# Kernel optimization log

Measured on AMD Instinct MI355X. Metric: run time of the kernel, lower is better.

## Reference

```python
import jax, jax.numpy as jnp
import numpy as np
from jax import lax

BITWIDTH = 7
EPS = 1e-5


def ti_quant(x):
    """TiFloatToInt8: per-tensor int8 quantization with power-of-2 scale."""
    rng = jnp.max(jnp.abs(x))
    bw = jnp.ceil(jnp.log2(rng))
    exp = bw - BITWIDTH
    q = jnp.clip(jnp.round(x * 2.0 ** (BITWIDTH - bw)), -128.0, 127.0)
    return q, exp


def ti_conv(xv, xe, wv, we, pad):
    """TiConv2d: integer conv (simulated in f32, all values int-valued),
    int32 accumulate, then shift back to 8 bits; exponents add."""
    acc = lax.conv_general_dilated(
        xv, wv, window_strides=(1, 1), padding=[(pad, pad), (pad, pad)],
        dimension_numbers=("NCHW", "OIHW", "NCHW"))
    rng = jnp.max(jnp.abs(acc))
    bw = jnp.ceil(jnp.log2(rng))
    shift = jnp.maximum(bw - BITWIDTH, 0.0)
    q = jnp.clip(jnp.round(acc * 2.0 ** (-shift)), -128.0, 127.0)
    return q, xe + we + shift


def batchnorm(x, gamma, beta):
    # training-mode BN: batch statistics over (N, H, W)
    mean = jnp.mean(x, axis=(0, 2, 3), keepdims=True)
    var = jnp.var(x, axis=(0, 2, 3), keepdims=True)
    g = gamma[None, :, None, None]
    b = beta[None, :, None, None]
    return g * (x - mean) * lax.rsqrt(var + EPS) + b


def setup_inputs() -> dict:
    key = jax.random.key(0)
    k0, k1, k2, k3, k4 = jax.random.split(key, 5)
    B, Cin, Cout, H, W = 32, 128, 256, 56, 56
    x_val = jax.random.randint(k0, (B, Cin, H, W), -128, 128, dtype=jnp.int32)
    x_exp = jnp.zeros((), jnp.float32) - 7.0
    wDW = jnp.round(jnp.clip(jax.random.normal(k1, (Cin, Cin, 3, 3), jnp.float32) * 32.0, -128.0, 127.0))
    wDW_exp = jnp.zeros((), jnp.float32) - 9.0
    wPW = jnp.round(jnp.clip(jax.random.normal(k2, (Cout, Cin, 1, 1), jnp.float32) * 32.0, -128.0, 127.0))
    wPW_exp = jnp.zeros((), jnp.float32) - 9.0
    gamma1 = jnp.ones((Cin,), jnp.float32) + 0.1 * jax.random.normal(k3, (Cin,), jnp.float32)
    beta1 = jnp.zeros((Cin,), jnp.float32)
    gamma2 = jnp.ones((Cout,), jnp.float32) + 0.1 * jax.random.normal(k4, (Cout,), jnp.float32)
    beta2 = jnp.zeros((Cout,), jnp.float32)
    return {"x_val": x_val, "x_exp": x_exp, "wDW": wDW, "wDW_exp": wDW_exp,
            "wPW": wPW, "wPW_exp": wPW_exp, "gamma1": gamma1, "beta1": beta1,
            "gamma2": gamma2, "beta2": beta2}


def reference(x_val, x_exp, wDW, wDW_exp, wPW, wPW_exp, gamma1, beta1, gamma2, beta2):
    xv = x_val.astype(jnp.float32)
    # convDW (3x3, in->in, pad=1)
    q, e = ti_conv(xv, x_exp, wDW, wDW_exp, 1)
    # dequant -> bn1 -> quant
    f = batchnorm(q * 2.0 ** e, gamma1, beta1)
    q, e = ti_quant(f)
    # TiReLU on int values
    q = jnp.maximum(q, 0.0)
    # convPW (1x1, in->out)
    q, e = ti_conv(q, e, wPW, wPW_exp, 0)
    # dequant -> bn2 -> quant -> relu
    f = batchnorm(q * 2.0 ** e, gamma2, beta2)
    q, e = ti_quant(f)
    q = jnp.maximum(q, 0.0)
    return q.astype(jnp.int8), e
```

## Files before the change

kernel.cpp:

```cpp
#include <hip/hip_runtime.h>
#include <cstdint>
#include <cstddef>

#define C1 128
#define C2 256
#define Hh 56
#define Wd 56
#define HW 3136
#define NHW 100352
#define N1 ((size_t)12845056)
#define N2 ((size_t)25690112)
#define XPSZ ((size_t)13778944)
#define NREP 8

typedef int v4i __attribute__((ext_vector_type(4)));
typedef int v16i __attribute__((ext_vector_type(16)));

static constexpr size_t OFF_XP = 0;
static constexpr size_t OFF_ACC1 = XPSZ;
static constexpr size_t OFF_Q1 = OFF_ACC1 + 4 * N1;
static constexpr size_t OFF_Q3 = OFF_Q1 + N1;
static constexpr size_t OFF_WQ1 = OFF_Q3 + N2;
static constexpr size_t OFF_WQ2 = OFF_WQ1 + 147456;
static constexpr size_t OFF_STATS = OFF_WQ2 + 32768;

struct Stats {
  int absmax1, absmax2, tick1, tick2;
  float scale1, e1, s2, e2;
  float scaleq2, e3, sf, ef;
  int sum1[NREP][C1]; unsigned sumsq1[NREP][C1];
  int min1[NREP][C1], max1[NREP][C1];
  float A1[C1], B1c[C1];
  int sum2[NREP][C2]; unsigned sumsq2[NREP][C2];
  int min2[NREP][C2], max2[NREP][C2];
  float A2[C2], B2c[C2];
};

__global__ __launch_bounds__(256) void k_pre(
    const int* __restrict__ x, signed char* __restrict__ xp,
    const float* __restrict__ wDW, signed char* __restrict__ wq1t,
    const float* __restrict__ wPW, signed char* __restrict__ wq2t,
    Stats* st) {
  __shared__ signed char lds[56 * 132];
  int t = threadIdx.x, bid = blockIdx.x;
  if (bid < 1856) {
    int hh = bid % 58, n = bid / 58;
    int* xpw = (int*)(xp + ((size_t)n * 58 + hh) * 7424);
    if (hh == 0 || hh == 57) {
      for (int o = t; o < 1856; o += 256) xpw[o] = 0;
      return;
    }
    int h = hh - 1;
    const int* xb = x + (size_t)n * C1 * HW + h * 56;
    for (int idx = t; idx < 7168; idx += 256) {
      int c = idx / 56, w = idx - c * 56;
      lds[w * 132 + c] = (signed char)xb[(size_t)c * HW + w];
    }
    __syncthreads();
    for (int o = t; o < 1856; o += 256) {
      int kb = o / 232, r = o - kb * 232, ww = r >> 2, cw = r & 3;
      int val = (ww == 0 || ww == 57) ? 0
                : *(const int*)&lds[(ww - 1) * 132 + kb * 16 + cw * 4];
      xpw[o] = val;
    }
    return;
  }
  if (bid < 2432) {
    int idx = (bid - 1856) * 256 + t;
    int co = idx / 1152, r = idx - co * 1152;
    int ci = r / 9, pos = r - ci * 9;
    int k = pos * 128 + ci;
    wq1t[(size_t)(k >> 4) * 2048 + co * 16 + (k & 15)] = (signed char)(int)wDW[idx];
    return;
  }
  if (bid < 2560) {
    int i = (bid - 2432) * 256 + t;
    int co = i >> 7, ci = i & 127;
    wq2t[(size_t)(ci >> 4) * 4096 + co * 16 + (ci & 15)] = (signed char)(int)wPW[i];
    return;
  }
  if (t == 0) { st->absmax1 = 0; st->absmax2 = 0; st->tick1 = 0; st->tick2 = 0; }
  for (int c = t; c < NREP * C1; c += 256) {
    ((int*)st->sum1)[c] = 0; ((unsigned*)st->sumsq1)[c] = 0u;
    ((int*)st->min1)[c] = 127; ((int*)st->max1)[c] = -128;
  }
  for (int c = t; c < NREP * C2; c += 256) {
    ((int*)st->sum2)[c] = 0; ((unsigned*)st->sumsq2)[c] = 0u;
    ((int*)st->min2)[c] = 127; ((int*)st->max2)[c] = -128;
  }
}

__device__ inline v4i ld16_lds(const signed char* p) {
  const int2* q = (const int2*)p;
  int2 lo = q[0], hi = q[1];
  v4i r; r[0] = lo.x; r[1] = lo.y; r[2] = hi.x; r[3] = hi.y;
  return r;
}

__device__ inline float bn_affine_v(int sum, unsigned sumsq, int mn, int mx,
                                    float g, float b, float e_in,
                                    float* Aout, float* Bout) {
  double meanq = (double)sum / (double)NHW;
  double varq = (double)sumsq / (double)NHW - meanq * meanq;
  float se = exp2f(e_in);
  float mean = (float)meanq * se;
  float var = (float)varq * se * se;
  float rsq = 1.0f / sqrtf(var + 1e-5f);
  float Avv = g * se * rsq;
  float Bvv = b - g * mean * rsq;
  *Aout = Avv; *Bout = Bvv;
  return fmaxf(fabsf(Avv * (float)mn + Bvv), fabsf(Avv * (float)mx + Bvv));
}

__global__ __launch_bounds__(256, 2) void k_conv1s(
    const signed char* __restrict__ xp, const signed char* __restrict__ wq1t,
    int* __restrict__ acc1, Stats* st) {
  __shared__ int reda[4];
  int t = threadIdx.x, lane = t & 63, wave = t >> 6;
  int half = lane >> 5, l31 = lane & 31;
  size_t g0 = (size_t)blockIdx.x * 256;

  const signed char* ab[2];
#pragma unroll
  for (int i = 0; i < 2; ++i) {
    size_t gm = g0 + wave * 64 + i * 32 + l31;
    int n = (int)(gm / HW);
    int p = (int)(gm - (size_t)n * HW);
    int h = p / 56, w = p - h * 56;
    ab[i] = xp + ((size_t)n * 58 + h) * 7424 + w * 16 + half * 928;
  }
  const signed char* bb[4];
#pragma unroll
  for (int j = 0; j < 4; ++j)
    bb[j] = wq1t + (size_t)(j * 32 + l31) * 16 + half * 2048;

  v16i a1[2][4];
#pragma unroll
  for (int i = 0; i < 2; ++i)
#pragma unroll
    for (int j = 0; j < 4; ++j)
#pragma unroll
      for (int r = 0; r < 16; ++r) a1[i][j][r] = 0;

#pragma unroll
  for (int pos = 0; pos < 9; ++pos) {
    int kh = pos / 3, kw = pos - kh * 3;
    const signed char* a0p = ab[0] + kh * 7424 + kw * 16;
    const signed char* a1p = ab[1] + kh * 7424 + kw * 16;
#pragma unroll
    for (int kb = 0; kb < 8; kb += 2) {
      v4i af0 = *(const v4i*)(a0p + kb * 928);
      v4i af1 = *(const v4i*)(a1p + kb * 928);
      v4i bf[4];
#pragma unroll
      for (int j = 0; j < 4; ++j)
        bf[j] = *(const v4i*)(bb[j] + pos * 16384 + kb * 2048);
#pragma unroll
      for (int j = 0; j < 4; ++j) {
        a1[0][j] = __builtin_amdgcn_mfma_i32_32x32x32_i8(af0, bf[j], a1[0][j], 0, 0, 0);
        a1[1][j] = __builtin_amdgcn_mfma_i32_32x32x32_i8(af1, bf[j], a1[1][j], 0, 0, 0);
      }
    }
  }

  int am = 0;
#pragma unroll
  for (int i = 0; i < 2; ++i)
#pragma unroll
    for (int j = 0; j < 4; ++j)
#pragma unroll
      for (int r = 0; r < 16; ++r) am = max(am, abs(a1[i][j][r]));
  for (int off = 32; off; off >>= 1) am = max(am, __shfl_down(am, off, 64));
  if (lane == 0) reda[wave] = am;
  __syncthreads();
  if (t == 0)
    atomicMax(&st->absmax1, max(max(reda[0], reda[1]), max(reda[2], reda[3])));

  int* ob = acc1 + (size_t)blockIdx.x * 32768;
#pragma unroll
  for (int i = 0; i < 2; ++i)
#pragma unroll
    for (int j = 0; j < 4; ++j)
#pragma unroll
      for (int reg = 0; reg < 16; ++reg)
        ob[(((wave * 2 + i) * 4 + j) * 16 + reg) * 64 + lane] = a1[i][j][reg];
}

__global__ __launch_bounds__(256, 2) void k_qstats1(
    const int* __restrict__ acc1, signed char* __restrict__ q1, Stats* st,
    const float* __restrict__ x_exp, const float* __restrict__ wDW_exp,
    const float* __restrict__ gamma1, const float* __restrict__ beta1) {
  __shared__ int qti[256 * 34];
  __shared__ int psum[C1], psq[C1], pmn[C1], pmx[C1];
  __shared__ float redc[2];
  __shared__ int lastf;
  signed char* qt = (signed char*)qti;
  int t = threadIdx.x, lane = t & 63, wave = t >> 6;
  int half = lane >> 5, l31 = lane & 31;
  int rep = blockIdx.x & (NREP - 1);

  if (t < C1) { psum[t] = 0; psq[t] = 0; pmn[t] = 127; pmx[t] = -128; }
  __syncthreads();

  int v1 = st->absmax1;
  int pw = 31 - __clz(v1 | 1);
  int bw = ((v1 & (v1 - 1)) == 0) ? pw : pw + 1;
  int sh = max(bw - 7, 0);
  float scale1 = exp2f((float)(-sh));
  float e1 = x_exp[0] + wDW_exp[0] + (float)sh;
  if (blockIdx.x == 0 && t == 0) st->e1 = e1;

  const int* ib = acc1 + (size_t)blockIdx.x * 32768;
#pragma unroll
  for (int j = 0; j < 4; ++j) {
    int sj = 0, sqj = 0, mnj = 127, mxj = -128;
    int c = j * 32 + l31;
#pragma unroll
    for (int i = 0; i < 2; ++i)
#pragma unroll
      for (int reg = 0; reg < 16; ++reg) {
        int av = ib[(((wave * 2 + i) * 4 + j) * 16 + reg) * 64 + lane];
        int row = (reg & 3) + 8 * (reg >> 2) + 4 * half;
        int pix = wave * 64 + i * 32 + row;
        float r = rintf((float)av * scale1);
        r = fminf(fmaxf(r, -128.f), 127.f);
        int qi = (int)r;
        qt[pix * 136 + c] = (signed char)qi;
        sj += qi; sqj += qi * qi; mnj = min(mnj, qi); mxj = max(mxj, qi);
      }
    sj += __shfl_down(sj, 32, 64);
    sqj += __shfl_down(sqj, 32, 64);
    mnj = min(mnj, __shfl_down(mnj, 32, 64));
    mxj = max(mxj, __shfl_down(mxj, 32, 64));
    if (half == 0) {
      atomicAdd(&psum[c], sj); atomicAdd(&psq[c], sqj);
      atomicMin(&pmn[c], mnj); atomicMax(&pmx[c], mxj);
    }
  }
  __syncthreads();
  if (t < C1) {
    atomicAdd(&st->sum1[rep][t], psum[t]);
    atomicAdd(&st->sumsq1[rep][t], (unsigned)psq[t]);
    atomicMin(&st->min1[rep][t], pmn[t]);
    atomicMax(&st->max1[rep][t], pmx[t]);
  }
  int* q1w = (int*)(q1 + (size_t)blockIdx.x * 256 * 128);
  for (int idx = t; idx < 8192; idx += 256)
    q1w[idx] = qti[(idx >> 5) * 34 + (idx & 31)];

  __syncthreads();
  if (t == 0) lastf = (atomicAdd(&st->tick1, 1) == 391);
  __syncthreads();
  if (lastf) {
    if (t < C1) {
      int sm = 0; unsigned sq = 0; int mn = 127, mx = -128;
#pragma unroll
      for (int r2 = 0; r2 < NREP; ++r2) {
        sm += atomicAdd(&st->sum1[r2][t], 0);
        sq += atomicAdd(&st->sumsq1[r2][t], 0u);
        mn = min(mn, atomicMin(&st->min1[r2][t], 127));
        mx = max(mx, atomicMax(&st->max1[r2][t], -128));
      }
      float cand = bn_affine_v(sm, sq, mn, mx, gamma1[t], beta1[t], e1,
                               &st->A1[t], &st->B1c[t]);
      for (int off = 32; off; off >>= 1) cand = fmaxf(cand, __shfl_down(cand, off, 64));
      if ((t & 63) == 0) redc[t >> 6] = cand;
    }
    __syncthreads();
    if (t == 0) {
      float rng = fmaxf(redc[0], redc[1]);
      float bwv = ceilf(log2f(rng));
      st->s2 = exp2f(7.0f - bwv);
      st->e2 = bwv - 7.0f;
    }
  }
}

template <int STORE>
__global__ __launch_bounds__(256, 2) void k_conv2t(
    const signed char* __restrict__ q1, const signed char* __restrict__ wq2t,
    signed char* __restrict__ q3, Stats* st, const float* __restrict__ wPW_exp,
    const float* __restrict__ gamma2, const float* __restrict__ beta2,
    float* __restrict__ out) {
  __shared__ __align__(16) signed char wq2s[32768];
  __shared__ int qti[128 * 34];
  __shared__ int psum[C2], psq[C2], pmn[C2], pmx[C2];
  __shared__ int reda[4];
  __shared__ float red2[4];
  __shared__ int lastf;
  signed char* qt = (signed char*)qti;

  int t = threadIdx.x, lane = t & 63, wave = t >> 6;
  int half = lane >> 5, l31 = lane & 31;
  size_t g0 = (size_t)blockIdx.x * 128;
  int rep = blockIdx.x & (NREP - 1);

  v4i wtmp[8];
#pragma unroll
  for (int i = 0; i < 8; ++i)
    wtmp[i] = *(const v4i*)(wq2t + i * 4096 + t * 16);
  const int* q1w = (const int*)(q1 + g0 * 128);
  int qv[16];
#pragma unroll
  for (int k = 0; k < 16; ++k) qv[k] = q1w[k * 256 + t];

  if (STORE) { psum[t] = 0; psq[t] = 0; pmn[t] = 127; pmx[t] = -128; }

  int c4 = t & 31;
  float Av[4], Bv[4];
#pragma unroll
  for (int jj = 0; jj < 4; ++jj) {
    Av[jj] = st->A1[c4 * 4 + jj];
    Bv[jj] = st->B1c[c4 * 4 + jj];
  }
  float s2 = st->s2;

#pragma unroll
  for (int i = 0; i < 8; ++i)
    *(v4i*)(wq2s + i * 4096 + t * 16) = wtmp[i];

#pragma unroll
  for (int k = 0; k < 16; ++k) {
    int v = qv[k];
    int pix = (k * 256 + t) >> 5;
    int outv = 0;
#pragma unroll
    for (int jj = 0; jj < 4; ++jj) {
      int b = (signed char)(v >> (8 * jj));
      float y = Av[jj] * (float)b + Bv[jj];
      float r = rintf(y * s2);
      r = fminf(fmaxf(r, -128.f), 127.f);
      r = fmaxf(r, 0.f);
      outv |= ((int)r & 0xff) << (8 * jj);
    }
    qti[pix * 34 + c4] = outv;
  }
  __syncthreads();

  v16i acc[8];
#pragma unroll
  for (int j = 0; j < 8; ++j)
#pragma unroll
    for (int r = 0; r < 16; ++r) acc[j][r] = 0;

#pragma unroll
  for (int ks = 0; ks < 4; ++ks) {
    v4i af = ld16_lds(&qt[(wave * 32 + l31) * 136 + half * 16 + ks * 32]);
#pragma unroll
    for (int j = 0; j < 8; ++j) {
      v4i bf = *(const v4i*)(wq2s + (size_t)(ks * 2 + half) * 4096 + (j * 32 + l31) * 16);
      acc[j] = __builtin_amdgcn_mfma_i32_32x32x32_i8(af, bf, acc[j], 0, 0, 0);
    }
  }

  if (STORE == 0) {
    int am2 = 0;
#pragma unroll
    for (int j = 0; j < 8; ++j)
#pragma unroll
      for (int r = 0; r < 16; ++r) am2 = max(am2, abs(acc[j][r]));
    for (int off = 32; off; off >>= 1) am2 = max(am2, __shfl_down(am2, off, 64));
    if (lane == 0) reda[wave] = am2;
    __syncthreads();
    if (t == 0)
      atomicMax(&st->absmax2, max(max(reda[0], reda[1]), max(reda[2], reda[3])));
  } else {
    int v2 = st->absmax2;
    int pw = 31 - __clz(v2 | 1);
    int bw = ((v2 & (v2 - 1)) == 0) ? pw : pw + 1;
    int sh2 = max(bw - 7, 0);
    float scale2 = exp2f((float)(-sh2));
    float e3 = st->e2 + wPW_exp[0] + (float)sh2;
    if (blockIdx.x == 0 && t == 0) st->e3 = e3;
    int* q3w = (int*)(q3 + (size_t)blockIdx.x * 32768);
#pragma unroll
    for (int j = 0; j < 8; ++j) {
      int c = j * 32 + l31;
      int sj = 0, sqj = 0, mnj = 127, mxj = -128;
#pragma unroll
      for (int rg = 0; rg < 4; ++rg) {
        int pk = 0;
#pragma unroll
        for (int b = 0; b < 4; ++b) {
          float r = rintf((float)acc[j][4 * rg + b] * scale2);
          r = fminf(fmaxf(r, -128.f), 127.f);
          int qi = (int)r;
          pk |= (qi & 0xff) << (8 * b);
          sj += qi; sqj += qi * qi; mnj = min(mnj, qi); mxj = max(mxj, qi);
        }
        q3w[((wave * 8 + j) * 4 + rg) * 64 + lane] = pk;
      }
      sj += __shfl_down(sj, 32, 64);
      sqj += __shfl_down(sqj, 32, 64);
      mnj = min(mnj, __shfl_down(mnj, 32, 64));
      mxj = max(mxj, __shfl_down(mxj, 32, 64));
      if (half == 0) {
        atomicAdd(&psum[c], sj); atomicAdd(&psq[c], sqj);
        atomicMin(&pmn[c], mnj); atomicMax(&pmx[c], mxj);
      }
    }
    __syncthreads();
    atomicAdd(&st->sum2[rep][t], psum[t]);
    atomicAdd(&st->sumsq2[rep][t], (unsigned)psq[t]);
    atomicMin(&st->min2[rep][t], pmn[t]);
    atomicMax(&st->max2[rep][t], pmx[t]);

    __syncthreads();
    if (t == 0) lastf = (atomicAdd(&st->tick2, 1) == 783);
    __syncthreads();
    if (lastf) {
      int sm = 0; unsigned sq = 0; int mn = 127, mx = -128;
#pragma unroll
      for (int r2 = 0; r2 < NREP; ++r2) {
        sm += atomicAdd(&st->sum2[r2][t], 0);
        sq += atomicAdd(&st->sumsq2[r2][t], 0u);
        mn = min(mn, atomicMin(&st->min2[r2][t], 127));
        mx = max(mx, atomicMax(&st->max2[r2][t], -128));
      }
      float cand = bn_affine_v(sm, sq, mn, mx, gamma2[t], beta2[t], e3,
                               &st->A2[t], &st->B2c[t]);
      for (int off = 32; off; off >>= 1) cand = fmaxf(cand, __shfl_down(cand, off, 64));
      if (lane == 0) red2[wave] = cand;
      __syncthreads();
      if (t == 0) {
        float rng = fmaxf(fmaxf(red2[0], red2[1]), fmaxf(red2[2], red2[3]));
        float bwv = ceilf(log2f(rng));
        st->sf = exp2f(7.0f - bwv);
        st->ef = bwv - 7.0f;
        out[N2] = bwv - 7.0f;
      }
    }
  }
}

__global__ __launch_bounds__(256) void k_out(
    const signed char* __restrict__ q3, const Stats* __restrict__ st,
    float* __restrict__ out) {
  __shared__ int ldsc[256 * 17];
  int t = threadIdx.x, lane = t & 63, wave = t >> 6;
  int bid = blockIdx.x;
  size_t g0 = (size_t)bid * 64;
  int n = (int)(g0 / HW), p0 = (int)(g0 - (size_t)n * HW);
  const int* q3r = (const int*)(q3 + (size_t)(bid >> 1) * 32768) + (bid & 1) * 4096;
#pragma unroll
  for (int k = 0; k < 16; ++k) {
    int i = k * 256 + t;
    int ln = i & 63, rg = (i >> 6) & 3, j = (i >> 8) & 7, wv = (i >> 11) & 1;
    int v = q3r[i];
    int c = j * 32 + (ln & 31);
    int psub = wv * 8 + 2 * rg + (ln >> 5);
    ldsc[c * 17 + psub] = v;
  }
  __syncthreads();
  float sf = st->sf;
  float* ob = out + (size_t)n * C2 * HW + p0 + lane;
#pragma unroll
  for (int cg = 0; cg < 64; ++cg) {
    int c = wave * 64 + ((cg + wave * 16) & 63);
    int vv = ldsc[c * 17 + (lane >> 2)];
    float y = st->A2[c] * (float)((signed char)(vv >> (8 * (lane & 3)))) + st->B2c[c];
    float r = rintf(y * sf);
    r = fminf(fmaxf(r, -128.f), 127.f);
    ob[(size_t)c * HW] = fmaxf(r, 0.f);
  }
}

extern "C" void kernel_launch(void* const* d_in, const int* in_sizes, int n_in,
                              void* d_out, int out_size, void* d_ws, size_t ws_size,
                              hipStream_t stream) {
  const int* x = (const int*)d_in[0];
  const float* x_exp = (const float*)d_in[1];
  const float* wDW = (const float*)d_in[2];
  const float* wDW_exp = (const float*)d_in[3];
  const float* wPW = (const float*)d_in[4];
  const float* wPW_exp = (const float*)d_in[5];
  const float* gamma1 = (const float*)d_in[6];
  const float* beta1 = (const float*)d_in[7];
  const float* gamma2 = (const float*)d_in[8];
  const float* beta2 = (const float*)d_in[9];
  float* out = (float*)d_out;

  char* ws = (char*)d_ws;
  signed char* xp2 = (signed char*)(ws + OFF_XP);
  int* acc1 = (int*)(ws + OFF_ACC1);
  signed char* q1 = (signed char*)(ws + OFF_Q1);
  signed char* q3 = (signed char*)(ws + OFF_Q3);
  signed char* wq1t = (signed char*)(ws + OFF_WQ1);
  signed char* wq2t = (signed char*)(ws + OFF_WQ2);
  Stats* st = (Stats*)(ws + OFF_STATS);

  hipLaunchKernelGGL(k_pre, dim3(2561), dim3(256), 0, stream,
                     x, xp2, wDW, wq1t, wPW, wq2t, st);
  hipLaunchKernelGGL(k_conv1s, dim3(392), dim3(256), 0, stream,
                     xp2, wq1t, acc1, st);
  hipLaunchKernelGGL(k_qstats1, dim3(392), dim3(256), 0, stream,
                     acc1, q1, st, x_exp, wDW_exp, gamma1, beta1);
  hipLaunchKernelGGL(HIP_KERNEL_NAME(k_conv2t<0>), dim3(784), dim3(256), 0, stream,
                     q1, wq2t, q3, st, wPW_exp, gamma2, beta2, out);
  hipLaunchKernelGGL(HIP_KERNEL_NAME(k_conv2t<1>), dim3(784), dim3(256), 0, stream,
                     q1, wq2t, q3, st, wPW_exp, gamma2, beta2, out);
  hipLaunchKernelGGL(k_out, dim3(1568), dim3(256), 0, stream, q3, st, out);
}
```

Baseline: 271.4 us.

## Recompute conv1 in stats kernel instead of storing int32 accumulators

The 3x3 conv MFMA loop is factored into a device function and run twice: once to find the global absmax, and again in the quantize/stats kernel. The int32 accumulator buffer is no longer written or read back, which removes about 100 MB of global memory traffic. The cost is doing the int8 conv MFMA work twice.

```diff
diff --git a/kernel.cpp b/kernel.cpp
--- a/kernel.cpp
+++ b/kernel.cpp
@@ -17,8 +17,7 @@
 typedef int v16i __attribute__((ext_vector_type(16)));
 
 static constexpr size_t OFF_XP = 0;
-static constexpr size_t OFF_ACC1 = XPSZ;
-static constexpr size_t OFF_Q1 = OFF_ACC1 + 4 * N1;
+static constexpr size_t OFF_Q1 = XPSZ;
 static constexpr size_t OFF_Q3 = OFF_Q1 + N1;
 static constexpr size_t OFF_WQ1 = OFF_Q3 + N2;
 static constexpr size_t OFF_WQ2 = OFF_WQ1 + 147456;
@@ -112,13 +111,12 @@
   return fmaxf(fabsf(Avv * (float)mn + Bvv), fabsf(Avv * (float)mx + Bvv));
 }
 
-__global__ __launch_bounds__(256, 2) void k_conv1s(
-    const signed char* __restrict__ xp, const signed char* __restrict__ wq1t,
-    int* __restrict__ acc1, Stats* st) {
-  __shared__ int reda[4];
-  int t = threadIdx.x, lane = t & 63, wave = t >> 6;
+__device__ inline void conv1_mfma(const signed char* __restrict__ xp,
+                                  const signed char* __restrict__ wq1t,
+                                  int bx, int t, v16i a1[2][4]) {
+  int lane = t & 63, wave = t >> 6;
   int half = lane >> 5, l31 = lane & 31;
-  size_t g0 = (size_t)blockIdx.x * 256;
+  size_t g0 = (size_t)bx * 256;
 
   const signed char* ab[2];
 #pragma unroll
@@ -134,7 +132,6 @@
   for (int j = 0; j < 4; ++j)
     bb[j] = wq1t + (size_t)(j * 32 + l31) * 16 + half * 2048;
 
-  v16i a1[2][4];
 #pragma unroll
   for (int i = 0; i < 2; ++i)
 #pragma unroll
@@ -162,6 +159,15 @@
       }
     }
   }
+}
+
+__global__ __launch_bounds__(256, 2) void k_conv1a(
+    const signed char* __restrict__ xp, const signed char* __restrict__ wq1t,
+    Stats* st) {
+  __shared__ int reda[4];
+  int t = threadIdx.x, lane = t & 63, wave = t >> 6;
+  v16i a1[2][4];
+  conv1_mfma(xp, wq1t, blockIdx.x, t, a1);
 
   int am = 0;
 #pragma unroll
@@ -175,19 +181,11 @@
   __syncthreads();
   if (t == 0)
     atomicMax(&st->absmax1, max(max(reda[0], reda[1]), max(reda[2], reda[3])));
-
-  int* ob = acc1 + (size_t)blockIdx.x * 32768;
-#pragma unroll
-  for (int i = 0; i < 2; ++i)
-#pragma unroll
-    for (int j = 0; j < 4; ++j)
-#pragma unroll
-      for (int reg = 0; reg < 16; ++reg)
-        ob[(((wave * 2 + i) * 4 + j) * 16 + reg) * 64 + lane] = a1[i][j][reg];
-}
-
-__global__ __launch_bounds__(256, 2) void k_qstats1(
-    const int* __restrict__ acc1, signed char* __restrict__ q1, Stats* st,
+}
+
+__global__ __launch_bounds__(256, 2) void k_conv1b(
+    const signed char* __restrict__ xp, const signed char* __restrict__ wq1t,
+    signed char* __restrict__ q1, Stats* st,
     const float* __restrict__ x_exp, const float* __restrict__ wDW_exp,
     const float* __restrict__ gamma1, const float* __restrict__ beta1) {
   __shared__ int qti[256 * 34];
@@ -199,6 +197,9 @@
   int half = lane >> 5, l31 = lane & 31;
   int rep = blockIdx.x & (NREP - 1);
 
+  v16i a1[2][4];
+  conv1_mfma(xp, wq1t, blockIdx.x, t, a1);
+
   if (t < C1) { psum[t] = 0; psq[t] = 0; pmn[t] = 127; pmx[t] = -128; }
   __syncthreads();
 
@@ -210,7 +211,6 @@
   float e1 = x_exp[0] + wDW_exp[0] + (float)sh;
   if (blockIdx.x == 0 && t == 0) st->e1 = e1;
 
-  const int* ib = acc1 + (size_t)blockIdx.x * 32768;
 #pragma unroll
   for (int j = 0; j < 4; ++j) {
     int sj = 0, sqj = 0, mnj = 127, mxj = -128;
@@ -219,7 +219,7 @@
     for (int i = 0; i < 2; ++i)
 #pragma unroll
       for (int reg = 0; reg < 16; ++reg) {
-        int av = ib[(((wave * 2 + i) * 4 + j) * 16 + reg) * 64 + lane];
+        int av = a1[i][j][reg];
         int row = (reg & 3) + 8 * (reg >> 2) + 4 * half;
         int pix = wave * 64 + i * 32 + row;
         float r = rintf((float)av * scale1);
@@ -482,7 +482,6 @@
 
   char* ws = (char*)d_ws;
   signed char* xp2 = (signed char*)(ws + OFF_XP);
-  int* acc1 = (int*)(ws + OFF_ACC1);
   signed char* q1 = (signed char*)(ws + OFF_Q1);
   signed char* q3 = (signed char*)(ws + OFF_Q3);
   signed char* wq1t = (signed char*)(ws + OFF_WQ1);
@@ -491,10 +490,10 @@
 
   hipLaunchKernelGGL(k_pre, dim3(2561), dim3(256), 0, stream,
                      x, xp2, wDW, wq1t, wPW, wq2t, st);
-  hipLaunchKernelGGL(k_conv1s, dim3(392), dim3(256), 0, stream,
-                     xp2, wq1t, acc1, st);
-  hipLaunchKernelGGL(k_qstats1, dim3(392), dim3(256), 0, stream,
-                     acc1, q1, st, x_exp, wDW_exp, gamma1, beta1);
+  hipLaunchKernelGGL(k_conv1a, dim3(392), dim3(256), 0, stream,
+                     xp2, wq1t, st);
+  hipLaunchKernelGGL(k_conv1b, dim3(392), dim3(256), 0, stream,
+                     xp2, wq1t, q1, st, x_exp, wDW_exp, gamma1, beta1);
   hipLaunchKernelGGL(HIP_KERNEL_NAME(k_conv2t<0>), dim3(784), dim3(256), 0, stream,
                      q1, wq2t, q3, st, wPW_exp, gamma2, beta2, out);
   hipLaunchKernelGGL(HIP_KERNEL_NAME(k_conv2t<1>), dim3(784), dim3(256), 0, stream,
```

After: 279.2 us. 1.03x slower.

## Cut LDS and register use in pointwise conv to raise occupancy

Applied to the files above, without the earlier changes.

The pointwise conv kernel no longer stages the 32 KB weight matrix in LDS. It reads B fragments directly from global memory and relies on cache hits instead. The output-channel loop is split into two halves of four accumulator tiles, which halves live accumulator registers. Both this kernel and the BN1 stats kernel now request four blocks per CU in their launch bounds. The trade is repeated global and L1 weight loads, plus e3 now being read back from global memory in the last block, in exchange for higher occupancy and latency hiding.

```diff
diff --git a/kernel.cpp b/kernel.cpp
--- a/kernel.cpp
+++ b/kernel.cpp
@@ -186,7 +186,7 @@
         ob[(((wave * 2 + i) * 4 + j) * 16 + reg) * 64 + lane] = a1[i][j][reg];
 }
 
-__global__ __launch_bounds__(256, 2) void k_qstats1(
+__global__ __launch_bounds__(256, 4) void k_qstats1(
     const int* __restrict__ acc1, signed char* __restrict__ q1, Stats* st,
     const float* __restrict__ x_exp, const float* __restrict__ wDW_exp,
     const float* __restrict__ gamma1, const float* __restrict__ beta1) {
@@ -277,12 +277,11 @@
 }
 
 template <int STORE>
-__global__ __launch_bounds__(256, 2) void k_conv2t(
+__global__ __launch_bounds__(256, 4) void k_conv2t(
     const signed char* __restrict__ q1, const signed char* __restrict__ wq2t,
     signed char* __restrict__ q3, Stats* st, const float* __restrict__ wPW_exp,
     const float* __restrict__ gamma2, const float* __restrict__ beta2,
     float* __restrict__ out) {
-  __shared__ __align__(16) signed char wq2s[32768];
   __shared__ int qti[128 * 34];
   __shared__ int psum[C2], psq[C2], pmn[C2], pmx[C2];
   __shared__ int reda[4];
@@ -295,15 +294,6 @@
   size_t g0 = (size_t)blockIdx.x * 128;
   int rep = blockIdx.x & (NREP - 1);
 
-  v4i wtmp[8];
-#pragma unroll
-  for (int i = 0; i < 8; ++i)
-    wtmp[i] = *(const v4i*)(wq2t + i * 4096 + t * 16);
-  const int* q1w = (const int*)(q1 + g0 * 128);
-  int qv[16];
-#pragma unroll
-  for (int k = 0; k < 16; ++k) qv[k] = q1w[k * 256 + t];
-
   if (STORE) { psum[t] = 0; psq[t] = 0; pmn[t] = 127; pmx[t] = -128; }
 
   int c4 = t & 31;
@@ -314,14 +304,10 @@
     Bv[jj] = st->B1c[c4 * 4 + jj];
   }
   float s2 = st->s2;
-
-#pragma unroll
-  for (int i = 0; i < 8; ++i)
-    *(v4i*)(wq2s + i * 4096 + t * 16) = wtmp[i];
-
+  const int* q1w = (const int*)(q1 + g0 * 128);
 #pragma unroll
   for (int k = 0; k < 16; ++k) {
-    int v = qv[k];
+    int v = q1w[k * 256 + t];
     int pix = (k * 256 + t) >> 5;
     int outv = 0;
 #pragma unroll
@@ -337,68 +323,81 @@
   }
   __syncthreads();
 
-  v16i acc[8];
-#pragma unroll
-  for (int j = 0; j < 8; ++j)
-#pragma unroll
-    for (int r = 0; r < 16; ++r) acc[j][r] = 0;
-
-#pragma unroll
-  for (int ks = 0; ks < 4; ++ks) {
-    v4i af = ld16_lds(&qt[(wave * 32 + l31) * 136 + half * 16 + ks * 32]);
-#pragma unroll
-    for (int j = 0; j < 8; ++j) {
-      v4i bf = *(const v4i*)(wq2s + (size_t)(ks * 2 + half) * 4096 + (j * 32 + l31) * 16);
-      acc[j] = __builtin_amdgcn_mfma_i32_32x32x32_i8(af, bf, acc[j], 0, 0, 0);
+  int sh2 = 0; float scale2 = 1.0f;
+  if (STORE) {
+    int v2 = st->absmax2;
+    int pw = 31 - __clz(v2 | 1);
+    int bw = ((v2 & (v2 - 1)) == 0) ? pw : pw + 1;
+    sh2 = max(bw - 7, 0);
+    scale2 = exp2f((float)(-sh2));
+    float e3 = st->e2 + wPW_exp[0] + (float)sh2;
+    if (blockIdx.x == 0 && t == 0) st->e3 = e3;
+  }
+
+  int am2 = 0;
+  int* q3w = (int*)(q3 + (size_t)blockIdx.x * 32768);
+#pragma unroll
+  for (int h2 = 0; h2 < 2; ++h2) {
+    v16i acc[4];
+#pragma unroll
+    for (int j = 0; j < 4; ++j)
+#pragma unroll
+      for (int r = 0; r < 16; ++r) acc[j][r] = 0;
+
+#pragma unroll
+    for (int ks = 0; ks < 4; ++ks) {
+      v4i af = ld16_lds(&qt[(wave * 32 + l31) * 136 + half * 16 + ks * 32]);
+#pragma unroll
+      for (int j = 0; j < 4; ++j) {
+        v4i bf = *(const v4i*)(wq2t + (size_t)(ks * 2 + half) * 4096 +
+                               ((h2 * 4 + j) * 32 + l31) * 16);
+        acc[j] = __builtin_amdgcn_mfma_i32_32x32x32_i8(af, bf, acc[j], 0, 0, 0);
+      }
+    }
+
+    if (STORE == 0) {
+#pragma unroll
+      for (int j = 0; j < 4; ++j)
+#pragma unroll
+        for (int r = 0; r < 16; ++r) am2 = max(am2, abs(acc[j][r]));
+    } else {
+#pragma unroll
+      for (int j = 0; j < 4; ++j) {
+        int jg = h2 * 4 + j;
+        int c = jg * 32 + l31;
+        int sj = 0, sqj = 0, mnj = 127, mxj = -128;
+#pragma unroll
+        for (int rg = 0; rg < 4; ++rg) {
+          int pk = 0;
+#pragma unroll
+          for (int b = 0; b < 4; ++b) {
+            float r = rintf((float)acc[j][4 * rg + b] * scale2);
+            r = fminf(fmaxf(r, -128.f), 127.f);
+            int qi = (int)r;
+            pk |= (qi & 0xff) << (8 * b);
+            sj += qi; sqj += qi * qi; mnj = min(mnj, qi); mxj = max(mxj, qi);
+          }
+          q3w[((wave * 8 + jg) * 4 + rg) * 64 + lane] = pk;
+        }
+        sj += __shfl_down(sj, 32, 64);
+        sqj += __shfl_down(sqj, 32, 64);
+        mnj = min(mnj, __shfl_down(mnj, 32, 64));
+        mxj = max(mxj, __shfl_down(mxj, 32, 64));
+        if (half == 0) {
+          atomicAdd(&psum[c], sj); atomicAdd(&psq[c], sqj);
+          atomicMin(&pmn[c], mnj); atomicMax(&pmx[c], mxj);
+        }
+      }
     }
   }
 
   if (STORE == 0) {
-    int am2 = 0;
-#pragma unroll
-    for (int j = 0; j < 8; ++j)
-#pragma unroll
-      for (int r = 0; r < 16; ++r) am2 = max(am2, abs(acc[j][r]));
     for (int off = 32; off; off >>= 1) am2 = max(am2, __shfl_down(am2, off, 64));
     if (lane == 0) reda[wave] = am2;
     __syncthreads();
     if (t == 0)
       atomicMax(&st->absmax2, max(max(reda[0], reda[1]), max(reda[2], reda[3])));
   } else {
-    int v2 = st->absmax2;
-    int pw = 31 - __clz(v2 | 1);
-    int bw = ((v2 & (v2 - 1)) == 0) ? pw : pw + 1;
-    int sh2 = max(bw - 7, 0);
-    float scale2 = exp2f((float)(-sh2));
-    float e3 = st->e2 + wPW_exp[0] + (float)sh2;
-    if (blockIdx.x == 0 && t == 0) st->e3 = e3;
-    int* q3w = (int*)(q3 + (size_t)blockIdx.x * 32768);
-#pragma unroll
-    for (int j = 0; j < 8; ++j) {
-      int c = j * 32 + l31;
-      int sj = 0, sqj = 0, mnj = 127, mxj = -128;
-#pragma unroll
-      for (int rg = 0; rg < 4; ++rg) {
-        int pk = 0;
-#pragma unroll
-        for (int b = 0; b < 4; ++b) {
-          float r = rintf((float)acc[j][4 * rg + b] * scale2);
-          r = fminf(fmaxf(r, -128.f), 127.f);
-          int qi = (int)r;
-          pk |= (qi & 0xff) << (8 * b);
-          sj += qi; sqj += qi * qi; mnj = min(mnj, qi); mxj = max(mxj, qi);
-        }
-        q3w[((wave * 8 + j) * 4 + rg) * 64 + lane] = pk;
-      }
-      sj += __shfl_down(sj, 32, 64);
-      sqj += __shfl_down(sqj, 32, 64);
-      mnj = min(mnj, __shfl_down(mnj, 32, 64));
-      mxj = max(mxj, __shfl_down(mxj, 32, 64));
-      if (half == 0) {
-        atomicAdd(&psum[c], sj); atomicAdd(&psq[c], sqj);
-        atomicMin(&pmn[c], mnj); atomicMax(&pmx[c], mxj);
-      }
-    }
     __syncthreads();
     atomicAdd(&st->sum2[rep][t], psum[t]);
     atomicAdd(&st->sumsq2[rep][t], (unsigned)psq[t]);
@@ -417,6 +416,7 @@
         mn = min(mn, atomicMin(&st->min2[r2][t], 127));
         mx = max(mx, atomicMax(&st->max2[r2][t], -128));
       }
+      float e3 = st->e3;
       float cand = bn_affine_v(sm, sq, mn, mx, gamma2[t], beta2[t], e3,
                                &st->A2[t], &st->B2c[t]);
       for (int off = 32; off; off >>= 1) cand = fmaxf(cand, __shfl_down(cand, off, 64));
```

New measurement: 274.2 us. About the same (+1.0%).
